# Optimization experiments

Measured on AMD Instinct MI355X. Metric: run time of the kernel, lower is better.

## Reference

```python
import jax, jax.numpy as jnp
import numpy as np

EPS = 1e-08  # attention offset, matches module epsilon


def _ln(x, g, b, eps=1e-5):
    m = jnp.mean(x, axis=-1, keepdims=True)
    v = jnp.var(x, axis=-1, keepdims=True)
    return (x - m) * jax.lax.rsqrt(v + eps) * g + b


def setup_inputs() -> dict:
    key = jax.random.key(0)
    ks = jax.random.split(key, 12)
    B, N, D, S, H = 32, 16384, 64, 7, 128
    sc = 1.0 / np.sqrt(D)
    sch = 1.0 / np.sqrt(H)
    return {
        "inputs": jax.random.normal(ks[0], (B, N, D), jnp.float32),
        "ln_in_g": jnp.ones((D,), jnp.float32), "ln_in_b": jnp.zeros((D,), jnp.float32),
        "ln_slots_g": jnp.ones((D,), jnp.float32), "ln_slots_b": jnp.zeros((D,), jnp.float32),
        "ln_mlp_g": jnp.ones((D,), jnp.float32), "ln_mlp_b": jnp.zeros((D,), jnp.float32),
        "Wq": jax.random.normal(ks[1], (D, D), jnp.float32) * sc,
        "Wk": jax.random.normal(ks[2], (D, D), jnp.float32) * sc,
        "Wv": jax.random.normal(ks[3], (D, D), jnp.float32) * sc,
        "slots_mu": jax.random.normal(ks[4], (1, 1, D), jnp.float32),
        "slots_log_sigma": jax.random.normal(ks[5], (1, 1, D), jnp.float32) * 0.1,
        "w_ih": jax.random.normal(ks[6], (3 * D, D), jnp.float32) * sc,
        "w_hh": jax.random.normal(ks[7], (3 * D, D), jnp.float32) * sc,
        "b_ih": jnp.zeros((3 * D,), jnp.float32), "b_hh": jnp.zeros((3 * D,), jnp.float32),
        "mlp_w1": jax.random.normal(ks[8], (H, D), jnp.float32) * sc,
        "mlp_b1": jnp.zeros((H,), jnp.float32),
        "mlp_w2": jax.random.normal(ks[9], (D, H), jnp.float32) * sch,
        "mlp_b2": jnp.zeros((D,), jnp.float32),
        "noise_slots": jax.random.normal(ks[10], (B, S, D), jnp.float32),
        "noise_h": jax.random.normal(ks[11], (B, D), jnp.float32),
        "num_iterations": 3,
    }


def reference(inputs, ln_in_g, ln_in_b, ln_slots_g, ln_slots_b, ln_mlp_g, ln_mlp_b,
              Wq, Wk, Wv, slots_mu, slots_log_sigma, w_ih, w_hh, b_ih, b_hh,
              mlp_w1, mlp_b1, mlp_w2, mlp_b2, noise_slots, noise_h, num_iterations):
    D = inputs.shape[-1]
    scale = D ** -0.5

    x = _ln(inputs, ln_in_g, ln_in_b)               # [B,N,D]
    k = jnp.einsum('bnd,ed->bne', x, Wk)            # [B,N,D]
    v = jnp.einsum('bnd,ed->bne', x, Wv)            # [B,N,D]

    sigma = jnp.exp(slots_log_sigma)
    slots = slots_mu + sigma * noise_slots          # [B,S,D]
    h0 = (slots_mu + sigma * noise_h[None])[0]      # [B,D] (torch h0 is [1,B,D])

    def gru_step(h, x_t):  # torch GRU cell, gate order r,z,n
        gi = x_t @ w_ih.T + b_ih
        gh = h @ w_hh.T + b_hh
        ir, iz, inn = jnp.split(gi, 3, axis=-1)
        hr, hz, hn = jnp.split(gh, 3, axis=-1)
        r = jax.nn.sigmoid(ir + hr)
        z = jax.nn.sigmoid(iz + hz)
        n = jnp.tanh(inn + r * hn)
        h_new = (1.0 - z) * n + z * h
        return h_new, h_new

    for _ in range(num_iterations):
        sn = _ln(slots, ln_slots_g, ln_slots_b)
        q = jnp.einsum('bsd,ed->bse', sn, Wq) * scale        # [B,S,D]
        logits = jnp.einsum('bnd,bsd->bns', k, q)            # [B,N,S]
        attn = jax.nn.softmax(logits, axis=-1) + EPS          # softmax over slots
        attn = attn / jnp.sum(attn, axis=1, keepdims=True)   # normalize over inputs (dim=-2)
        updates = jnp.einsum('bns,bnd->bsd', attn, v)        # [B,S,D]
        # nn.GRU over the slot axis as "time", fixed h0 each iteration
        _, hs = jax.lax.scan(gru_step, h0, jnp.swapaxes(updates, 0, 1))
        slots = jnp.swapaxes(hs, 0, 1)                       # [B,S,D]
        hid = jax.nn.relu(_ln(slots, ln_mlp_g, ln_mlp_b) @ mlp_w1.T + mlp_b1)
        slots = slots + (hid @ mlp_w2.T + mlp_b2)
    return slots
```

## Files before the change

kernel.cpp:

```cpp
#include <hip/hip_runtime.h>
#include <hip/hip_bf16.h>


#define B_ 32
#define N_ 16384
#define D_ 64
#define S_ 7

typedef __bf16 bf16x8 __attribute__((ext_vector_type(8)));
typedef float floatx4 __attribute__((ext_vector_type(4)));

__device__ __forceinline__ unsigned int f2bfu(float f) {
  __hip_bfloat16 h = __float2bfloat16(f);
  return (unsigned int)__builtin_bit_cast(unsigned short, h);
}
__device__ __forceinline__ unsigned int pack2bf(float lo, float hi) {
  return f2bfu(lo) | (f2bfu(hi) << 16);
}

__global__ __launch_bounds__(256) void proj_kernel(
    const float* __restrict__ x,
    const float* __restrict__ lng, const float* __restrict__ lnb,
    const float* __restrict__ Wk, const float* __restrict__ Wv,
    unsigned short* __restrict__ kb, unsigned short* __restrict__ vt)
{
  __shared__ __align__(16) unsigned char smem[32768];
  unsigned short* s_xn = (unsigned short*)smem;
  unsigned short* s_w  = (unsigned short*)(smem + 16384);
  unsigned short* s_ko = (unsigned short*)smem;
  unsigned short* s_vo = (unsigned short*)smem;

  const int t = threadIdx.x, lane = t & 63, w = t >> 6;
  const int R0 = blockIdx.x * 128;
  const int bb = R0 >> 14;
  const int nbase = R0 & (N_ - 1);

#pragma unroll
  for (int p = 0; p < 4; ++p) {
    int idx = (p * 256 + t) * 8;
    const float* src = (idx < 4096) ? (Wk + idx) : (Wv + idx - 4096);
    float4 a = ((const float4*)src)[0], b = ((const float4*)src)[1];
    uint4 pk;
    pk.x = pack2bf(a.x, a.y); pk.y = pack2bf(a.z, a.w);
    pk.z = pack2bf(b.x, b.y); pk.w = pack2bf(b.z, b.w);
    *(uint4*)&s_w[idx] = pk;
  }

  const int ql = t & 3;
  float4 g4[4], b4[4];
#pragma unroll
  for (int j = 0; j < 4; ++j) {
    g4[j] = *(const float4*)&lng[ql * 16 + j * 4];
    b4[j] = *(const float4*)&lnb[ql * 16 + j * 4];
  }
#pragma unroll
  for (int half = 0; half < 2; ++half) {
    int r = half * 64 + (t >> 2);
    const float4* xp = (const float4*)&x[(size_t)(R0 + r) * 64 + ql * 16];
    float4 xv[4];
#pragma unroll
    for (int j = 0; j < 4; ++j) xv[j] = xp[j];
    float s1 = 0.f, s2 = 0.f;
#pragma unroll
    for (int j = 0; j < 4; ++j) {
      s1 += xv[j].x + xv[j].y + xv[j].z + xv[j].w;
      s2 += xv[j].x * xv[j].x + xv[j].y * xv[j].y + xv[j].z * xv[j].z + xv[j].w * xv[j].w;
    }
    s1 += __shfl_xor(s1, 1); s2 += __shfl_xor(s2, 1);
    s1 += __shfl_xor(s1, 2); s2 += __shfl_xor(s2, 2);
    float mean = s1 * 0.015625f;
    float var = s2 * 0.015625f - mean * mean;
    float rs = rsqrtf(var + 1e-5f);
    float y[16];
#pragma unroll
    for (int j = 0; j < 4; ++j) {
      y[j * 4 + 0] = (xv[j].x - mean) * rs * g4[j].x + b4[j].x;
      y[j * 4 + 1] = (xv[j].y - mean) * rs * g4[j].y + b4[j].y;
      y[j * 4 + 2] = (xv[j].z - mean) * rs * g4[j].z + b4[j].z;
      y[j * 4 + 3] = (xv[j].w - mean) * rs * g4[j].w + b4[j].w;
    }
#pragma unroll
    for (int h = 0; h < 2; ++h) {
      uint4 p;
      p.x = pack2bf(y[h * 8 + 0], y[h * 8 + 1]);
      p.y = pack2bf(y[h * 8 + 2], y[h * 8 + 3]);
      p.z = pack2bf(y[h * 8 + 4], y[h * 8 + 5]);
      p.w = pack2bf(y[h * 8 + 6], y[h * 8 + 7]);
      int c = ql * 2 + h;
      int sc = c ^ (r & 7);
      *(uint4*)&s_xn[r * 64 + sc * 8] = p;
    }
  }
  __syncthreads();

  const int m16 = lane & 15, quad = lane >> 4;
  bf16x8 bf[2][2];
#pragma unroll
  for (int rt = 0; rt < 2; ++rt) {
    int xr = (w * 2 + rt) * 16 + m16;
#pragma unroll
    for (int kk = 0; kk < 2; ++kk)
      bf[rt][kk] = *(const bf16x8*)&s_xn[xr * 64 + (((kk * 4 + quad) ^ (xr & 7)) * 8)];
  }
  bf16x8 wkf[4][2], wvf[4][2];
#pragma unroll
  for (int ft = 0; ft < 4; ++ft)
#pragma unroll
    for (int kk = 0; kk < 2; ++kk) {
      wkf[ft][kk] = *(const bf16x8*)&s_w[(ft * 16 + m16) * 64 + kk * 32 + quad * 8];
      wvf[ft][kk] = *(const bf16x8*)&s_w[(64 + ft * 16 + m16) * 64 + kk * 32 + quad * 8];
    }
  __syncthreads();

#pragma unroll
  for (int ft = 0; ft < 4; ++ft)
#pragma unroll
    for (int rt = 0; rt < 2; ++rt) {
      floatx4 acc = (floatx4){0.f, 0.f, 0.f, 0.f};
      acc = __builtin_amdgcn_mfma_f32_16x16x32_bf16(wkf[ft][0], bf[rt][0], acc, 0, 0, 0);
      acc = __builtin_amdgcn_mfma_f32_16x16x32_bf16(wkf[ft][1], bf[rt][1], acc, 0, 0, 0);
      int n_l = (w * 2 + rt) * 16 + m16;
      uint2 p;
      p.x = pack2bf(acc[0], acc[1]);
      p.y = pack2bf(acc[2], acc[3]);
      *(uint2*)&s_ko[n_l * 72 + ft * 16 + quad * 4] = p;
    }
  __syncthreads();
#pragma unroll
  for (int p = 0; p < 4; ++p) {
    int ii = (p * 256 + t) * 8;
    int n_l = ii >> 6, dl = ii & 63;
    uint4 v4 = *(const uint4*)&s_ko[n_l * 72 + dl];
    *(uint4*)&kb[(size_t)(R0 + n_l) * 64 + dl] = v4;
  }
  __syncthreads();

#pragma unroll
  for (int ft = 0; ft < 4; ++ft)
#pragma unroll
    for (int rt = 0; rt < 2; ++rt) {
      floatx4 acc = (floatx4){0.f, 0.f, 0.f, 0.f};
      acc = __builtin_amdgcn_mfma_f32_16x16x32_bf16(bf[rt][0], wvf[ft][0], acc, 0, 0, 0);
      acc = __builtin_amdgcn_mfma_f32_16x16x32_bf16(bf[rt][1], wvf[ft][1], acc, 0, 0, 0);
      int n_l = (w * 2 + rt) * 16 + quad * 4;
      int d0 = ft * 16 + m16;
      uint2 p;
      p.x = pack2bf(acc[0], acc[1]);
      p.y = pack2bf(acc[2], acc[3]);
      *(uint2*)&s_vo[d0 * 136 + n_l] = p;
    }
  __syncthreads();
#pragma unroll
  for (int p = 0; p < 4; ++p) {
    int ii = (p * 256 + t) * 8;
    int d0 = ii >> 7, nl = ii & 127;
    uint4 v4 = *(const uint4*)&s_vo[d0 * 136 + nl];
    *(uint4*)&vt[((size_t)bb * 64 + d0) * N_ + nbase + nl] = v4;
  }
}

__device__ void q_from_slots(const float* s_slot, float* s_tmp,
                             const float* __restrict__ g, const float* __restrict__ bb,
                             const float* __restrict__ Wq, float* __restrict__ qout,
                             int lane, int w)
{
  for (int ss = 0; ss < 2; ++ss) {
    int srow = ss * 4 + w;
    if (srow < 7) {
      float xv = s_slot[srow * 64 + lane];
      float s1 = xv, s2 = xv * xv;
#pragma unroll
      for (int mm = 1; mm < 64; mm <<= 1) {
        s1 += __shfl_xor(s1, mm);
        s2 += __shfl_xor(s2, mm);
      }
      float mean = s1 * 0.015625f;
      float var = s2 * 0.015625f - mean * mean;
      float rs = rsqrtf(var + 1e-5f);
      s_tmp[w * 64 + lane] = (xv - mean) * rs * g[lane] + bb[lane];
    }
    __syncthreads();
    if (srow < 7) {
      float acc = 0.f;
      const float4* wr = (const float4*)(Wq + lane * 64);
      const float4* xr = (const float4*)(s_tmp + w * 64);
#pragma unroll
      for (int i = 0; i < 16; ++i) {
        float4 a = wr[i], xx = xr[i];
        acc += a.x * xx.x + a.y * xx.y + a.z * xx.z + a.w * xx.w;
      }
      qout[srow * 64 + lane] = acc * 0.125f;
    }
    __syncthreads();
  }
}

__global__ __launch_bounds__(256) void init_kernel(
    const float* __restrict__ mu, const float* __restrict__ lsig,
    const float* __restrict__ nslots, const float* __restrict__ nh,
    const float* __restrict__ ln_s_g, const float* __restrict__ ln_s_b,
    const float* __restrict__ Wq,
    float* __restrict__ qbuf, float* __restrict__ Wacc, float* __restrict__ Cacc,
    float* __restrict__ h0b)
{
  __shared__ float s_slot[448];
  __shared__ float s_tmp[256];
  const int b = blockIdx.x, t = threadIdx.x, lane = t & 63, w = t >> 6;
  for (int o = t; o < 448; o += 256) {
    int d = o & 63;
    s_slot[o] = mu[d] + expf(lsig[d]) * nslots[b * 448 + o];
    Wacc[b * 448 + o] = 0.f;
  }
  if (t < 64) h0b[b * 64 + t] = mu[t] + expf(lsig[t]) * nh[b * 64 + t];
  if (t < 8) Cacc[b * 8 + t] = 0.f;
  __syncthreads();
  q_from_slots(s_slot, s_tmp, ln_s_g, ln_s_b, Wq, qbuf + b * 448, lane, w);
}

__global__ __launch_bounds__(256) void attn_kernel(
    const unsigned short* __restrict__ kb, const unsigned short* __restrict__ vt,
    const float* __restrict__ qbuf,
    float* __restrict__ Wacc, float* __restrict__ Cacc)
{
  __shared__ __align__(16) unsigned short s_qb[16 * 64];
  __shared__ __align__(16) unsigned short s_at[4][16 * 136];
  __shared__ __align__(16) float s_red[4][448];
  __shared__ float s_cred[4][8];

  const int b = blockIdx.y;
  const int t = threadIdx.x, lane = t & 63, w = t >> 6;
  const int m16 = lane & 15, quad = lane >> 4;

  {
    int i0 = t * 4;
    int s = i0 >> 6, d0 = i0 & 63;
    float f0 = 0.f, f1 = 0.f, f2 = 0.f, f3 = 0.f;
    if (s < 7) {
      const float* qp = qbuf + b * 448 + s * 64 + d0;
      f0 = qp[0]; f1 = qp[1]; f2 = qp[2]; f3 = qp[3];
    }
    uint2 p;
    p.x = pack2bf(f0, f1);
    p.y = pack2bf(f2, f3);
    *(uint2*)&s_qb[i0] = p;
  }
  __syncthreads();

  bf16x8 bq0 = *(const bf16x8*)&s_qb[m16 * 64 + quad * 8];
  bf16x8 bq1 = *(const bf16x8*)&s_qb[m16 * 64 + 32 + quad * 8];

  const int n0w = blockIdx.x * 512 + w * 128;
  const unsigned short* kbA = kb + ((size_t)b * N_ + n0w) * 64;

  float cl = 0.f;
#pragma unroll
  for (int nt = 0; nt < 8; ++nt) {
    bf16x8 a0 = *(const bf16x8*)&kbA[(size_t)(nt * 16 + m16) * 64 + quad * 8];
    bf16x8 a1 = *(const bf16x8*)&kbA[(size_t)(nt * 16 + m16) * 64 + 32 + quad * 8];
    floatx4 c = (floatx4){0.f, 0.f, 0.f, 0.f};
    c = __builtin_amdgcn_mfma_f32_16x16x32_bf16(a0, bq0, c, 0, 0, 0);
    c = __builtin_amdgcn_mfma_f32_16x16x32_bf16(a1, bq1, c, 0, 0, 0);
    float atv[4];
#pragma unroll
    for (int rg = 0; rg < 4; ++rg) {
      float xx = (m16 < 7) ? c[rg] : -1e30f;
      float mx = xx;
      mx = fmaxf(mx, __shfl_xor(mx, 1));
      mx = fmaxf(mx, __shfl_xor(mx, 2));
      mx = fmaxf(mx, __shfl_xor(mx, 4));
      float e = __expf(xx - mx);
      float sm = e;
      sm += __shfl_xor(sm, 1);
      sm += __shfl_xor(sm, 2);
      sm += __shfl_xor(sm, 4);
      float a = e / sm + 1e-8f;
      atv[rg] = a;
      cl += a;
    }
    if (m16 < 7) {
      uint2 p;
      p.x = pack2bf(atv[0], atv[1]);
      p.y = pack2bf(atv[2], atv[3]);
      *(uint2*)&s_at[w][m16 * 136 + nt * 16 + quad * 4] = p;
    }
  }
  asm volatile("s_waitcnt lgkmcnt(0)" ::: "memory");

  floatx4 acc[4];
#pragma unroll
  for (int dt = 0; dt < 4; ++dt) acc[dt] = (floatx4){0.f, 0.f, 0.f, 0.f};
  const unsigned short* vtB = vt + (size_t)b * 64 * N_ + n0w;
#pragma unroll
  for (int ch = 0; ch < 4; ++ch) {
    bf16x8 af = *(const bf16x8*)&s_at[w][m16 * 136 + ch * 32 + quad * 8];
#pragma unroll
    for (int dt = 0; dt < 4; ++dt) {
      bf16x8 bv = *(const bf16x8*)&vtB[(size_t)(dt * 16 + m16) * N_ + ch * 32 + quad * 8];
      acc[dt] = __builtin_amdgcn_mfma_f32_16x16x32_bf16(af, bv, acc[dt], 0, 0, 0);
    }
  }
  if (quad < 2) {
#pragma unroll
    for (int dt = 0; dt < 4; ++dt)
#pragma unroll
      for (int rg = 0; rg < 4; ++rg) {
        int s = quad * 4 + rg;
        if (s < 7) s_red[w][s * 64 + dt * 16 + m16] = acc[dt][rg];
      }
  }
  cl += __shfl_xor(cl, 16);
  cl += __shfl_xor(cl, 32);
  if (m16 < 7 && quad == 0) s_cred[w][m16] = cl;
  __syncthreads();
  if (w == 0) {
#pragma unroll
    for (int s = 0; s < 7; ++s) {
      float v = s_red[0][s * 64 + lane] + s_red[1][s * 64 + lane] +
                s_red[2][s * 64 + lane] + s_red[3][s * 64 + lane];
      atomicAdd(&Wacc[b * 448 + s * 64 + lane], v);
    }
    if (lane < 7) {
      float c = s_cred[0][lane] + s_cred[1][lane] + s_cred[2][lane] + s_cred[3][lane];
      atomicAdd(&Cacc[b * 8 + lane], c);
    }
  }
}

__global__ __launch_bounds__(256) void slot_update_kernel(
    float* __restrict__ Wacc, float* __restrict__ Cacc,
    const float* __restrict__ h0b,
    const float* __restrict__ w_ih, const float* __restrict__ w_hh,
    const float* __restrict__ b_ih, const float* __restrict__ b_hh,
    const float* __restrict__ ln_m_g, const float* __restrict__ ln_m_b,
    const float* __restrict__ w1, const float* __restrict__ b1,
    const float* __restrict__ w2, const float* __restrict__ b2,
    const float* __restrict__ ln_s_g, const float* __restrict__ ln_s_b,
    const float* __restrict__ Wq,
    float* __restrict__ qbuf, float* __restrict__ out)
{
  const int b = blockIdx.x, t = threadIdx.x, lane = t & 63, w = t >> 6;
  __shared__ float s_whhT[64 * 201];
  __shared__ float s_upd[448];
  __shared__ float s_gi[1344];
  __shared__ float s_h[64];
  __shared__ float s_gh[192];
  __shared__ float s_slot[448];
  __shared__ float s_tmp[256];

  for (int i = t; i < 12288; i += 256) {
    int j = i >> 6, d = i & 63;
    s_whhT[d * 201 + j] = w_hh[i];
  }
  for (int o = t; o < 448; o += 256) {
    int s = o >> 6;
    s_upd[o] = Wacc[b * 448 + o] / Cacc[b * 8 + s];
  }
  if (t < 64) s_h[t] = h0b[b * 64 + t];
  __syncthreads();
  for (int o = t; o < 1344; o += 256) {
    int s = o / 192, j = o - s * 192;
    float acc = b_ih[j];
    const float4* wr = (const float4*)(w_ih + j * 64);
    const float4* ur = (const float4*)(s_upd + s * 64);
#pragma unroll
    for (int i = 0; i < 16; ++i) {
      float4 a = wr[i], u = ur[i];
      acc += a.x * u.x + a.y * u.y + a.z * u.z + a.w * u.w;
    }
    s_gi[o] = acc;
  }
  __syncthreads();
  for (int s = 0; s < 7; ++s) {
    if (t < 192) {
      float acc = b_hh[t];
#pragma unroll 16
      for (int d = 0; d < 64; ++d) acc += s_h[d] * s_whhT[d * 201 + t];
      s_gh[t] = acc;
    }
    __syncthreads();
    if (t < 64) {
      float ir = s_gi[s * 192 + t], iz = s_gi[s * 192 + 64 + t], inn = s_gi[s * 192 + 128 + t];
      float hr = s_gh[t], hz = s_gh[64 + t], hn = s_gh[128 + t];
      float r = 1.f / (1.f + expf(-(ir + hr)));
      float z = 1.f / (1.f + expf(-(iz + hz)));
      float n = tanhf(inn + r * hn);
      float hnew = (1.f - z) * n + z * s_h[t];
      s_slot[s * 64 + t] = hnew;
      s_h[t] = hnew;
    }
    __syncthreads();
  }
  float* s_sn = s_gi;
  float* s_hid = s_gi + 448;
  for (int ss = 0; ss < 2; ++ss) {
    int srow = ss * 4 + w;
    if (srow < 7) {
      float xv = s_slot[srow * 64 + lane];
      float s1 = xv, s2 = xv * xv;
#pragma unroll
      for (int mm = 1; mm < 64; mm <<= 1) {
        s1 += __shfl_xor(s1, mm);
        s2 += __shfl_xor(s2, mm);
      }
      float mean = s1 * 0.015625f;
      float var = s2 * 0.015625f - mean * mean;
      float rs = rsqrtf(var + 1e-5f);
      s_sn[srow * 64 + lane] = (xv - mean) * rs * ln_m_g[lane] + ln_m_b[lane];
    }
  }
  __syncthreads();
  for (int o = t; o < 896; o += 256) {
    int s = o >> 7, hh = o & 127;
    float acc = b1[hh];
    const float4* wr = (const float4*)(w1 + hh * 64);
    const float4* xr = (const float4*)(s_sn + s * 64);
#pragma unroll
    for (int i = 0; i < 16; ++i) {
      float4 a = wr[i], xx = xr[i];
      acc += a.x * xx.x + a.y * xx.y + a.z * xx.z + a.w * xx.w;
    }
    s_hid[o] = fmaxf(acc, 0.f);
  }
  __syncthreads();
  for (int o = t; o < 448; o += 256) {
    int s = o >> 6, d = o & 63;
    float acc = b2[d];
    const float4* wr = (const float4*)(w2 + d * 128);
    const float4* hr = (const float4*)(s_hid + s * 128);
#pragma unroll
    for (int i = 0; i < 32; ++i) {
      float4 a = wr[i], hv = hr[i];
      acc += a.x * hv.x + a.y * hv.y + a.z * hv.z + a.w * hv.w;
    }
    float val = s_slot[o] + acc;
    s_slot[o] = val;
    out[b * 448 + o] = val;
  }
  for (int o = t; o < 448; o += 256) Wacc[b * 448 + o] = 0.f;
  if (t < 8) Cacc[b * 8 + t] = 0.f;
  __syncthreads();
  q_from_slots(s_slot, s_tmp, ln_s_g, ln_s_b, Wq, qbuf + b * 448, lane, w);
}

extern "C" void kernel_launch(void* const* d_in, const int* in_sizes, int n_in,
                              void* d_out, int out_size, void* d_ws, size_t ws_size,
                              hipStream_t stream)
{
  (void)in_sizes; (void)n_in; (void)out_size; (void)ws_size;
  const float* x      = (const float*)d_in[0];
  const float* ln_in_g = (const float*)d_in[1];
  const float* ln_in_b = (const float*)d_in[2];
  const float* ln_s_g  = (const float*)d_in[3];
  const float* ln_s_b  = (const float*)d_in[4];
  const float* ln_m_g  = (const float*)d_in[5];
  const float* ln_m_b  = (const float*)d_in[6];
  const float* Wq = (const float*)d_in[7];
  const float* Wk = (const float*)d_in[8];
  const float* Wv = (const float*)d_in[9];
  const float* mu = (const float*)d_in[10];
  const float* lsig = (const float*)d_in[11];
  const float* w_ih = (const float*)d_in[12];
  const float* w_hh = (const float*)d_in[13];
  const float* b_ih = (const float*)d_in[14];
  const float* b_hh = (const float*)d_in[15];
  const float* w1 = (const float*)d_in[16];
  const float* b1 = (const float*)d_in[17];
  const float* w2 = (const float*)d_in[18];
  const float* b2 = (const float*)d_in[19];
  const float* nslots = (const float*)d_in[20];
  const float* nh = (const float*)d_in[21];

  unsigned short* kb = (unsigned short*)d_ws;
  unsigned short* vt = kb + (size_t)B_ * N_ * D_;
  float* fb = (float*)(vt + (size_t)B_ * N_ * D_);
  float* qbuf = fb;
  float* Wacc = fb + 14336;
  float* Cacc = fb + 28672;
  float* h0b  = fb + 28928;
  float* out = (float*)d_out;

  proj_kernel<<<4096, 256, 0, stream>>>(x, ln_in_g, ln_in_b, Wk, Wv, kb, vt);
  init_kernel<<<32, 256, 0, stream>>>(mu, lsig, nslots, nh, ln_s_g, ln_s_b, Wq,
                                      qbuf, Wacc, Cacc, h0b);
  for (int it = 0; it < 3; ++it) {
    attn_kernel<<<dim3(32, 32), 256, 0, stream>>>(kb, vt, qbuf, Wacc, Cacc);
    slot_update_kernel<<<32, 256, 0, stream>>>(Wacc, Cacc, h0b, w_ih, w_hh, b_ih, b_hh,
                                               ln_m_g, ln_m_b, w1, b1, w2, b2,
                                               ln_s_g, ln_s_b, Wq, qbuf, out);
  }
}
```

Baseline: 423.5 us.

## Precompute bf16 weights once, drop LDS staging in projection, retile attention kernel

Adds a one-block kernel that converts Wk/Wv to bf16 once, so each projection block reads them straight from global memory instead of converting and staging them in shared memory. The projection now issues both row loads up front and writes K and V^T outputs directly from MFMA registers, dropping the shared-memory transpose stages and their barriers. The attention kernel swaps MFMA operand order so slots sit on rows, computes the softmax with a single cross-half shuffle, halves the per-wave tile, and doubles the grid. GRU activations switch to fast exp-based sigmoid/tanh. Direct uint2 stores are less coalesced than the old uint4 staged stores, and the bigger grid doubles the atomic traffic.

```diff
diff --git a/kernel.cpp b/kernel.cpp
--- a/kernel.cpp
+++ b/kernel.cpp
@@ -17,24 +17,18 @@
 __device__ __forceinline__ unsigned int pack2bf(float lo, float hi) {
   return f2bfu(lo) | (f2bfu(hi) << 16);
 }
-
-__global__ __launch_bounds__(256) void proj_kernel(
-    const float* __restrict__ x,
-    const float* __restrict__ lng, const float* __restrict__ lnb,
+__device__ __forceinline__ float sigmoid_f(float x) {
+  return 1.f / (1.f + __expf(-x));
+}
+__device__ __forceinline__ float tanh_f(float x) {
+  return 1.f - 2.f / (1.f + __expf(2.f * x));
+}
+
+__global__ __launch_bounds__(256) void wconv_kernel(
     const float* __restrict__ Wk, const float* __restrict__ Wv,
-    unsigned short* __restrict__ kb, unsigned short* __restrict__ vt)
-{
-  __shared__ __align__(16) unsigned char smem[32768];
-  unsigned short* s_xn = (unsigned short*)smem;
-  unsigned short* s_w  = (unsigned short*)(smem + 16384);
-  unsigned short* s_ko = (unsigned short*)smem;
-  unsigned short* s_vo = (unsigned short*)smem;
-
-  const int t = threadIdx.x, lane = t & 63, w = t >> 6;
-  const int R0 = blockIdx.x * 128;
-  const int bb = R0 >> 14;
-  const int nbase = R0 & (N_ - 1);
-
+    unsigned short* __restrict__ wbf)
+{
+  const int t = threadIdx.x;
 #pragma unroll
   for (int p = 0; p < 4; ++p) {
     int idx = (p * 256 + t) * 8;
@@ -43,23 +37,44 @@
     uint4 pk;
     pk.x = pack2bf(a.x, a.y); pk.y = pack2bf(a.z, a.w);
     pk.z = pack2bf(b.x, b.y); pk.w = pack2bf(b.z, b.w);
-    *(uint4*)&s_w[idx] = pk;
-  }
+    *(uint4*)&wbf[idx] = pk;
+  }
+}
+
+__global__ __launch_bounds__(256) void proj_kernel(
+    const float* __restrict__ x,
+    const float* __restrict__ lng, const float* __restrict__ lnb,
+    const unsigned short* __restrict__ wbf,
+    unsigned short* __restrict__ kb, unsigned short* __restrict__ vt)
+{
+  __shared__ __align__(16) unsigned short s_xn[128 * 64];
+  const int t = threadIdx.x, lane = t & 63, w = t >> 6;
+  const int R0 = blockIdx.x * 128;
+  const int bb = R0 >> 14;
+  const int nbase = R0 & (N_ - 1);
 
   const int ql = t & 3;
+  const int r0r = t >> 2;
+  float4 xv0[4], xv1[4];
+  {
+    const float4* xp0 = (const float4*)&x[(size_t)(R0 + r0r) * 64 + ql * 16];
+    const float4* xp1 = (const float4*)&x[(size_t)(R0 + 64 + r0r) * 64 + ql * 16];
+#pragma unroll
+    for (int j = 0; j < 4; ++j) xv0[j] = xp0[j];
+#pragma unroll
+    for (int j = 0; j < 4; ++j) xv1[j] = xp1[j];
+  }
   float4 g4[4], b4[4];
 #pragma unroll
   for (int j = 0; j < 4; ++j) {
     g4[j] = *(const float4*)&lng[ql * 16 + j * 4];
     b4[j] = *(const float4*)&lnb[ql * 16 + j * 4];
   }
+
 #pragma unroll
   for (int half = 0; half < 2; ++half) {
-    int r = half * 64 + (t >> 2);
-    const float4* xp = (const float4*)&x[(size_t)(R0 + r) * 64 + ql * 16];
-    float4 xv[4];
-#pragma unroll
-    for (int j = 0; j < 4; ++j) xv[j] = xp[j];
+    int r = half * 64 + r0r;
+    float4* xv = half ? xv1 : xv0;
     float s1 = 0.f, s2 = 0.f;
 #pragma unroll
     for (int j = 0; j < 4; ++j) {
@@ -102,60 +117,41 @@
     for (int kk = 0; kk < 2; ++kk)
       bf[rt][kk] = *(const bf16x8*)&s_xn[xr * 64 + (((kk * 4 + quad) ^ (xr & 7)) * 8)];
   }
-  bf16x8 wkf[4][2], wvf[4][2];
-#pragma unroll
-  for (int ft = 0; ft < 4; ++ft)
-#pragma unroll
-    for (int kk = 0; kk < 2; ++kk) {
-      wkf[ft][kk] = *(const bf16x8*)&s_w[(ft * 16 + m16) * 64 + kk * 32 + quad * 8];
-      wvf[ft][kk] = *(const bf16x8*)&s_w[(64 + ft * 16 + m16) * 64 + kk * 32 + quad * 8];
-    }
-  __syncthreads();
-
-#pragma unroll
-  for (int ft = 0; ft < 4; ++ft)
+
+#pragma unroll
+  for (int ft = 0; ft < 4; ++ft) {
+    bf16x8 wk0 = *(const bf16x8*)&wbf[(ft * 16 + m16) * 64 + quad * 8];
+    bf16x8 wk1 = *(const bf16x8*)&wbf[(ft * 16 + m16) * 64 + 32 + quad * 8];
 #pragma unroll
     for (int rt = 0; rt < 2; ++rt) {
       floatx4 acc = (floatx4){0.f, 0.f, 0.f, 0.f};
-      acc = __builtin_amdgcn_mfma_f32_16x16x32_bf16(wkf[ft][0], bf[rt][0], acc, 0, 0, 0);
-      acc = __builtin_amdgcn_mfma_f32_16x16x32_bf16(wkf[ft][1], bf[rt][1], acc, 0, 0, 0);
+      acc = __builtin_amdgcn_mfma_f32_16x16x32_bf16(wk0, bf[rt][0], acc, 0, 0, 0);
+      acc = __builtin_amdgcn_mfma_f32_16x16x32_bf16(wk1, bf[rt][1], acc, 0, 0, 0);
       int n_l = (w * 2 + rt) * 16 + m16;
+      int d0 = ft * 16 + quad * 4;
       uint2 p;
       p.x = pack2bf(acc[0], acc[1]);
       p.y = pack2bf(acc[2], acc[3]);
-      *(uint2*)&s_ko[n_l * 72 + ft * 16 + quad * 4] = p;
-    }
-  __syncthreads();
-#pragma unroll
-  for (int p = 0; p < 4; ++p) {
-    int ii = (p * 256 + t) * 8;
-    int n_l = ii >> 6, dl = ii & 63;
-    uint4 v4 = *(const uint4*)&s_ko[n_l * 72 + dl];
-    *(uint4*)&kb[(size_t)(R0 + n_l) * 64 + dl] = v4;
-  }
-  __syncthreads();
-
-#pragma unroll
-  for (int ft = 0; ft < 4; ++ft)
+      *(uint2*)&kb[(size_t)(R0 + n_l) * 64 + d0] = p;
+    }
+  }
+
+#pragma unroll
+  for (int ft = 0; ft < 4; ++ft) {
+    bf16x8 wv0 = *(const bf16x8*)&wbf[(64 + ft * 16 + m16) * 64 + quad * 8];
+    bf16x8 wv1 = *(const bf16x8*)&wbf[(64 + ft * 16 + m16) * 64 + 32 + quad * 8];
 #pragma unroll
     for (int rt = 0; rt < 2; ++rt) {
       floatx4 acc = (floatx4){0.f, 0.f, 0.f, 0.f};
-      acc = __builtin_amdgcn_mfma_f32_16x16x32_bf16(bf[rt][0], wvf[ft][0], acc, 0, 0, 0);
-      acc = __builtin_amdgcn_mfma_f32_16x16x32_bf16(bf[rt][1], wvf[ft][1], acc, 0, 0, 0);
-      int n_l = (w * 2 + rt) * 16 + quad * 4;
+      acc = __builtin_amdgcn_mfma_f32_16x16x32_bf16(bf[rt][0], wv0, acc, 0, 0, 0);
+      acc = __builtin_amdgcn_mfma_f32_16x16x32_bf16(bf[rt][1], wv1, acc, 0, 0, 0);
+      int n_l = nbase + (w * 2 + rt) * 16 + quad * 4;
       int d0 = ft * 16 + m16;
       uint2 p;
       p.x = pack2bf(acc[0], acc[1]);
       p.y = pack2bf(acc[2], acc[3]);
-      *(uint2*)&s_vo[d0 * 136 + n_l] = p;
-    }
-  __syncthreads();
-#pragma unroll
-  for (int p = 0; p < 4; ++p) {
-    int ii = (p * 256 + t) * 8;
-    int d0 = ii >> 7, nl = ii & 127;
-    uint4 v4 = *(const uint4*)&s_vo[d0 * 136 + nl];
-    *(uint4*)&vt[((size_t)bb * 64 + d0) * N_ + nbase + nl] = v4;
+      *(uint2*)&vt[((size_t)bb * 64 + d0) * N_ + n_l] = p;
+    }
   }
 }
 
@@ -223,7 +219,7 @@
     float* __restrict__ Wacc, float* __restrict__ Cacc)
 {
   __shared__ __align__(16) unsigned short s_qb[16 * 64];
-  __shared__ __align__(16) unsigned short s_at[4][16 * 136];
+  __shared__ __align__(16) unsigned short s_at[4][16 * 72];
   __shared__ __align__(16) float s_red[4][448];
   __shared__ float s_cred[4][8];
 
@@ -246,42 +242,37 @@
   }
   __syncthreads();
 
-  bf16x8 bq0 = *(const bf16x8*)&s_qb[m16 * 64 + quad * 8];
-  bf16x8 bq1 = *(const bf16x8*)&s_qb[m16 * 64 + 32 + quad * 8];
-
-  const int n0w = blockIdx.x * 512 + w * 128;
-  const unsigned short* kbA = kb + ((size_t)b * N_ + n0w) * 64;
-
-  float cl = 0.f;
-#pragma unroll
-  for (int nt = 0; nt < 8; ++nt) {
-    bf16x8 a0 = *(const bf16x8*)&kbA[(size_t)(nt * 16 + m16) * 64 + quad * 8];
-    bf16x8 a1 = *(const bf16x8*)&kbA[(size_t)(nt * 16 + m16) * 64 + 32 + quad * 8];
+  bf16x8 aq0 = *(const bf16x8*)&s_qb[m16 * 64 + quad * 8];
+  bf16x8 aq1 = *(const bf16x8*)&s_qb[m16 * 64 + 32 + quad * 8];
+
+  const int n0g = blockIdx.x * 256 + w * 64;
+  const unsigned short* kbA = kb + ((size_t)b * N_ + n0g) * 64;
+
+  float clp[4] = {0.f, 0.f, 0.f, 0.f};
+
+#pragma unroll
+  for (int nt = 0; nt < 4; ++nt) {
+    bf16x8 bk0 = *(const bf16x8*)&kbA[(size_t)(nt * 16 + m16) * 64 + quad * 8];
+    bf16x8 bk1 = *(const bf16x8*)&kbA[(size_t)(nt * 16 + m16) * 64 + 32 + quad * 8];
     floatx4 c = (floatx4){0.f, 0.f, 0.f, 0.f};
-    c = __builtin_amdgcn_mfma_f32_16x16x32_bf16(a0, bq0, c, 0, 0, 0);
-    c = __builtin_amdgcn_mfma_f32_16x16x32_bf16(a1, bq1, c, 0, 0, 0);
-    float atv[4];
-#pragma unroll
-    for (int rg = 0; rg < 4; ++rg) {
-      float xx = (m16 < 7) ? c[rg] : -1e30f;
-      float mx = xx;
-      mx = fmaxf(mx, __shfl_xor(mx, 1));
-      mx = fmaxf(mx, __shfl_xor(mx, 2));
-      mx = fmaxf(mx, __shfl_xor(mx, 4));
-      float e = __expf(xx - mx);
-      float sm = e;
-      sm += __shfl_xor(sm, 1);
-      sm += __shfl_xor(sm, 2);
-      sm += __shfl_xor(sm, 4);
-      float a = e / sm + 1e-8f;
-      atv[rg] = a;
-      cl += a;
-    }
-    if (m16 < 7) {
-      uint2 p;
-      p.x = pack2bf(atv[0], atv[1]);
-      p.y = pack2bf(atv[2], atv[3]);
-      *(uint2*)&s_at[w][m16 * 136 + nt * 16 + quad * 4] = p;
+    c = __builtin_amdgcn_mfma_f32_16x16x32_bf16(aq0, bk0, c, 0, 0, 0);
+    c = __builtin_amdgcn_mfma_f32_16x16x32_bf16(aq1, bk1, c, 0, 0, 0);
+    float v0 = c[0], v1 = c[1], v2 = c[2], v3 = c[3];
+    if (quad == 1) v3 = -1e30f;
+    float mx = fmaxf(fmaxf(v0, v1), fmaxf(v2, v3));
+    float M = fmaxf(mx, __shfl_xor(mx, 16));
+    float e0 = __expf(v0 - M), e1 = __expf(v1 - M), e2 = __expf(v2 - M), e3 = __expf(v3 - M);
+    float s4 = e0 + e1 + e2 + e3;
+    float tot = s4 + __shfl_xor(s4, 16);
+    float inv = 1.f / tot;
+    float a0 = e0 * inv + 1e-8f, a1 = e1 * inv + 1e-8f;
+    float a2 = e2 * inv + 1e-8f, a3 = e3 * inv + 1e-8f;
+    if (quad < 2) {
+      clp[0] += a0; clp[1] += a1; clp[2] += a2; clp[3] += a3;
+      s_at[w][(quad * 4 + 0) * 72 + nt * 16 + m16] = (unsigned short)f2bfu(a0);
+      s_at[w][(quad * 4 + 1) * 72 + nt * 16 + m16] = (unsigned short)f2bfu(a1);
+      s_at[w][(quad * 4 + 2) * 72 + nt * 16 + m16] = (unsigned short)f2bfu(a2);
+      if (quad == 0) s_at[w][3 * 72 + nt * 16 + m16] = (unsigned short)f2bfu(a3);
     }
   }
   asm volatile("s_waitcnt lgkmcnt(0)" ::: "memory");
@@ -289,10 +280,10 @@
   floatx4 acc[4];
 #pragma unroll
   for (int dt = 0; dt < 4; ++dt) acc[dt] = (floatx4){0.f, 0.f, 0.f, 0.f};
-  const unsigned short* vtB = vt + (size_t)b * 64 * N_ + n0w;
-#pragma unroll
-  for (int ch = 0; ch < 4; ++ch) {
-    bf16x8 af = *(const bf16x8*)&s_at[w][m16 * 136 + ch * 32 + quad * 8];
+  const unsigned short* vtB = vt + (size_t)b * 64 * N_ + n0g;
+#pragma unroll
+  for (int ch = 0; ch < 2; ++ch) {
+    bf16x8 af = *(const bf16x8*)&s_at[w][m16 * 72 + ch * 32 + quad * 8];
 #pragma unroll
     for (int dt = 0; dt < 4; ++dt) {
       bf16x8 bv = *(const bf16x8*)&vtB[(size_t)(dt * 16 + m16) * N_ + ch * 32 + quad * 8];
@@ -308,9 +299,22 @@
         if (s < 7) s_red[w][s * 64 + dt * 16 + m16] = acc[dt][rg];
       }
   }
-  cl += __shfl_xor(cl, 16);
-  cl += __shfl_xor(cl, 32);
-  if (m16 < 7 && quad == 0) s_cred[w][m16] = cl;
+#pragma unroll
+  for (int rg = 0; rg < 4; ++rg) {
+    float c = clp[rg];
+    c += __shfl_xor(c, 1);
+    c += __shfl_xor(c, 2);
+    c += __shfl_xor(c, 4);
+    c += __shfl_xor(c, 8);
+    clp[rg] = c;
+  }
+  if (m16 == 0 && quad < 2) {
+#pragma unroll
+    for (int rg = 0; rg < 4; ++rg) {
+      int s = quad * 4 + rg;
+      if (s < 7) s_cred[w][s] = clp[rg];
+    }
+  }
   __syncthreads();
   if (w == 0) {
 #pragma unroll
@@ -381,9 +385,9 @@
     if (t < 64) {
       float ir = s_gi[s * 192 + t], iz = s_gi[s * 192 + 64 + t], inn = s_gi[s * 192 + 128 + t];
       float hr = s_gh[t], hz = s_gh[64 + t], hn = s_gh[128 + t];
-      float r = 1.f / (1.f + expf(-(ir + hr)));
-      float z = 1.f / (1.f + expf(-(iz + hz)));
-      float n = tanhf(inn + r * hn);
+      float r = sigmoid_f(ir + hr);
+      float z = sigmoid_f(iz + hz);
+      float n = tanh_f(inn + r * hn);
       float hnew = (1.f - z) * n + z * s_h[t];
       s_slot[s * 64 + t] = hnew;
       s_h[t] = hnew;
@@ -477,13 +481,15 @@
   float* Wacc = fb + 14336;
   float* Cacc = fb + 28672;
   float* h0b  = fb + 28928;
+  unsigned short* wbf = (unsigned short*)(fb + 30976);
   float* out = (float*)d_out;
 
-  proj_kernel<<<4096, 256, 0, stream>>>(x, ln_in_g, ln_in_b, Wk, Wv, kb, vt);
+  wconv_kernel<<<1, 256, 0, stream>>>(Wk, Wv, wbf);
+  proj_kernel<<<4096, 256, 0, stream>>>(x, ln_in_g, ln_in_b, wbf, kb, vt);
   init_kernel<<<32, 256, 0, stream>>>(mu, lsig, nslots, nh, ln_s_g, ln_s_b, Wq,
                                       qbuf, Wacc, Cacc, h0b);
   for (int it = 0; it < 3; ++it) {
-    attn_kernel<<<dim3(32, 32), 256, 0, stream>>>(kb, vt, qbuf, Wacc, Cacc);
+    attn_kernel<<<dim3(64, 32), 256, 0, stream>>>(kb, vt, qbuf, Wacc, Cacc);
     slot_update_kernel<<<32, 256, 0, stream>>>(Wacc, Cacc, h0b, w_ih, w_hh, b_ih, b_hh,
                                                ln_m_g, ln_m_b, w1, b1, w2, b2,
                                                ln_s_g, ln_s_b, Wq, qbuf, out);
```

After: 445.9 us. +5.3%, slower.
